# Kernel optimization log

Hardware: AMD Instinct MI355X
Metric: run time of the kernel (lower is better)

The kernel has to match this reference:

```python
import jax, jax.numpy as jnp
import numpy as np
import math

N_EMBD = 1024
N_HEAD = 16
HEAD_DIM = N_EMBD // N_HEAD // 2  # 32
DEPTH = 1
LAMBDA_INIT = 0.8 - 0.6 * math.exp(-0.3 * (DEPTH - 1))  # 0.2
EPS = 1e-5


def setup_inputs() -> dict:
    key = jax.random.key(0)
    ks = jax.random.split(key, 8)
    B, T, C = 4, 1024, N_EMBD
    x = jax.random.normal(ks[0], (B, T, C), dtype=jnp.float32)
    w_attn = jax.random.normal(ks[1], (C, 3 * C), dtype=jnp.float32) * (1.0 / math.sqrt(C))
    w_proj = jax.random.normal(ks[2], (C, C), dtype=jnp.float32) * (1.0 / math.sqrt(C))
    lambda_q1 = jax.random.normal(ks[3], (HEAD_DIM,), dtype=jnp.float32) * 0.1
    lambda_q2 = jax.random.normal(ks[4], (HEAD_DIM,), dtype=jnp.float32) * 0.1
    lambda_k1 = jax.random.normal(ks[5], (HEAD_DIM,), dtype=jnp.float32) * 0.1
    lambda_k2 = jax.random.normal(ks[6], (HEAD_DIM,), dtype=jnp.float32) * 0.1
    gamma = jnp.ones((2 * HEAD_DIM,), dtype=jnp.float32)  # RMSNorm affine weight
    return {"x": x, "w_attn": w_attn, "w_proj": w_proj,
            "lambda_q1": lambda_q1, "lambda_q2": lambda_q2,
            "lambda_k1": lambda_k1, "lambda_k2": lambda_k2, "gamma": gamma}


def reference(x, w_attn, w_proj, lambda_q1, lambda_q2, lambda_k1, lambda_k2, gamma):
    B, T, C = x.shape
    H, hd = N_HEAD, HEAD_DIM
    qkv = x @ w_attn                                  # [B,T,3C]
    q, k, v = jnp.split(qkv, 3, axis=-1)
    q = q.reshape(B, T, 2 * H, hd).transpose(0, 2, 1, 3)   # [B,2H,T,hd]
    k = k.reshape(B, T, 2 * H, hd).transpose(0, 2, 1, 3)   # [B,2H,T,hd]
    v = v.reshape(B, T, H, 2 * hd).transpose(0, 2, 1, 3)   # [B,H,T,2hd]
    q = q * (hd ** -0.5)
    att = jnp.einsum('bhtd,bhsd->bhts', q, k) * (1.0 / math.sqrt(hd))
    causal = jnp.tril(jnp.ones((T, T), dtype=bool))
    att = jnp.where(causal, att, -jnp.inf)
    att = jax.nn.softmax(att, axis=-1)                # [B,2H,T,T]
    lam1 = jnp.exp(jnp.sum(lambda_q1 * lambda_k1))
    lam2 = jnp.exp(jnp.sum(lambda_q2 * lambda_k2))
    lambda_full = lam1 - lam2 + LAMBDA_INIT
    att = att.reshape(B, H, 2, T, T)
    att = att[:, :, 0] - lambda_full * att[:, :, 1]   # [B,H,T,T]
    out = jnp.einsum('bhts,bhsd->bhtd', att, v)       # [B,H,T,2hd]
    # RMSNorm over last dim with affine weight
    rms = jax.lax.rsqrt(jnp.mean(out * out, axis=-1, keepdims=True) + EPS)
    out = out * rms * gamma
    out = (1.0 - LAMBDA_INIT) * out
    out = out.transpose(0, 2, 1, 3).reshape(B, T, C)
    return out @ w_proj
```

## Files before the change

### kernel.cpp

```cpp
#include <hip/hip_runtime.h>

typedef unsigned short u16;
typedef __bf16 bf16x8 __attribute__((ext_vector_type(8)));
typedef float f32x4 __attribute__((ext_vector_type(4)));
typedef u16 u16x8 __attribute__((ext_vector_type(8)));
typedef u16 u16x4 __attribute__((ext_vector_type(4)));

#define DEV static __device__ __forceinline__

DEV u16 f2bf(float f) {
  unsigned u = __builtin_bit_cast(unsigned, f);
  u += 0x7fffu + ((u >> 16) & 1u);
  return (u16)(u >> 16);
}
DEV u16 f2bf_fast(float f) {
  unsigned u = __builtin_bit_cast(unsigned, f);
  return (u16)((u + 0x8000u) >> 16);
}
DEV float fexp2(float x) {
  float r;
  asm("v_exp_f32 %0, %1" : "=v"(r) : "v"(x));
  return r;
}

DEV void gld16(const void* g, void* l) {
  __builtin_amdgcn_global_load_lds((__attribute__((address_space(1))) void*)(g),
                                   (__attribute__((address_space(3))) void*)(l),
                                   16, 0, 0);
}

__global__ __launch_bounds__(256) void k_cast(const float* __restrict__ in,
                                              u16* __restrict__ out, int n4) {
  int i = blockIdx.x * 256 + threadIdx.x;
  if (i >= n4) return;
  float4 v = ((const float4*)in)[i];
  u16x4 r = { f2bf(v.x), f2bf(v.y), f2bf(v.z), f2bf(v.w) };
  ((u16x4*)out)[i] = r;
}

__global__ __launch_bounds__(256) void k_transpose_cast(const float* __restrict__ in,
                                                        u16* __restrict__ out,
                                                        int R, int Cc) {
  __shared__ u16 tile[64][65];
  int r0 = blockIdx.x * 64, c0 = blockIdx.y * 64;
  int tid = threadIdx.x;
#pragma unroll
  for (int rr = 0; rr < 4; ++rr) {
    int r = rr * 16 + (tid >> 4);
    int c = (tid & 15) * 4;
    float4 v = *(const float4*)&in[(size_t)(r0 + r) * Cc + c0 + c];
    tile[r][c + 0] = f2bf(v.x); tile[r][c + 1] = f2bf(v.y);
    tile[r][c + 2] = f2bf(v.z); tile[r][c + 3] = f2bf(v.w);
  }
  __syncthreads();
#pragma unroll
  for (int rr = 0; rr < 2; ++rr) {
    int cr = rr * 32 + (tid >> 3);
    int rc = (tid & 7) * 8;
    u16x8 v;
#pragma unroll
    for (int j = 0; j < 8; ++j) v[j] = tile[rc + j][cr];
    *(u16x8*)&out[(size_t)(c0 + cr) * R + r0 + rc] = v;
  }
}

__global__ __launch_bounds__(256) void k_vtrans(const u16* __restrict__ qkv,
                                                u16* __restrict__ vt) {
  __shared__ u16 tile[64][65];
  int bid = blockIdx.x;
  int b = bid >> 8, h = (bid >> 4) & 15, tt = bid & 15;
  int tid = threadIdx.x;
#pragma unroll
  for (int rr = 0; rr < 2; ++rr) {
    int tl = rr * 32 + (tid >> 3);
    int d0 = (tid & 7) * 8;
    u16x8 v = *(const u16x8*)&qkv[(size_t)(b * 1024 + tt * 64 + tl) * 3072 + 2048 + h * 64 + d0];
#pragma unroll
    for (int j = 0; j < 8; ++j) tile[tl][d0 + j] = v[j];
  }
  __syncthreads();
#pragma unroll
  for (int rr = 0; rr < 2; ++rr) {
    int d = rr * 32 + (tid >> 3);
    int t0 = (tid & 7) * 8;
    u16x8 v;
#pragma unroll
    for (int j = 0; j < 8; ++j) v[j] = tile[t0 + j][d];
    *(u16x8*)&vt[((size_t)(b * 16 + h) * 64 + d) * 1024 + tt * 64 + t0] = v;
  }
}

__global__ void k_lambda(const float* lq1, const float* lq2,
                         const float* lk1, const float* lk2, float* out) {
  int i = threadIdx.x;
  float a = 0.f, b = 0.f;
  if (i < 32) { a = lq1[i] * lk1[i]; b = lq2[i] * lk2[i]; }
#pragma unroll
  for (int s = 1; s < 64; s <<= 1) { a += __shfl_xor(a, s); b += __shfl_xor(b, s); }
  if (i == 0) out[0] = __expf(a) - __expf(b) + 0.2f;
}

template <bool OUT_F32>
__global__ __launch_bounds__(256) void k_gemm(const u16* __restrict__ A,
                                              const u16* __restrict__ Bt,
                                              void* __restrict__ Cout,
                                              int M, int N, int K) {
  __shared__ __align__(16) u16 As[128 * 32];
  __shared__ __align__(16) u16 Bs[128 * 32];
  int tid = threadIdx.x;
  int nbn = N >> 7;
  int bm = blockIdx.x / nbn, bn = blockIdx.x % nbn;
  int m0 = bm << 7, n0 = bn << 7;
  int lane = tid & 63, w = tid >> 6, wm = w >> 1, wn = w & 1;
  int lr = lane & 15, lg = lane >> 4;
  f32x4 acc[4][4] = {};
  for (int kt = 0; kt < K; kt += 32) {
#pragma unroll
    for (int rr = 0; rr < 2; ++rr) {
      int i = rr * 256 + tid;
      int r = i >> 2, c8 = i & 3;
      int s8 = c8 ^ ((r >> 1) & 3);
      gld16(&A[(size_t)(m0 + r) * K + kt + s8 * 8], &As[i * 8]);
    }
#pragma unroll
    for (int rr = 0; rr < 2; ++rr) {
      int i = rr * 256 + tid;
      int r = i >> 2, c8 = i & 3;
      int s8 = c8 ^ ((r >> 1) & 3);
      gld16(&Bt[(size_t)(n0 + r) * K + kt + s8 * 8], &Bs[i * 8]);
    }
    __syncthreads();
    bf16x8 af[4], bfr[4];
#pragma unroll
    for (int m = 0; m < 4; ++m) {
      int r = wm * 64 + m * 16 + lr;
      int c8 = lg ^ ((r >> 1) & 3);
      af[m] = *(const bf16x8*)&As[r * 32 + c8 * 8];
    }
#pragma unroll
    for (int n = 0; n < 4; ++n) {
      int r = wn * 64 + n * 16 + lr;
      int c8 = lg ^ ((r >> 1) & 3);
      bfr[n] = *(const bf16x8*)&Bs[r * 32 + c8 * 8];
    }
#pragma unroll
    for (int m = 0; m < 4; ++m)
#pragma unroll
      for (int n = 0; n < 4; ++n)
        acc[m][n] = __builtin_amdgcn_mfma_f32_16x16x32_bf16(af[m], bfr[n], acc[m][n], 0, 0, 0);
    __syncthreads();
  }
#pragma unroll
  for (int m = 0; m < 4; ++m)
#pragma unroll
    for (int r = 0; r < 4; ++r) {
      int gr = m0 + wm * 64 + m * 16 + lg * 4 + r;
#pragma unroll
      for (int n = 0; n < 4; ++n) {
        int gc = n0 + wn * 64 + n * 16 + lr;
        if (OUT_F32) ((float*)Cout)[(size_t)gr * N + gc] = acc[m][n][r];
        else ((u16*)Cout)[(size_t)gr * N + gc] = f2bf(acc[m][n][r]);
      }
    }
}

__global__ __launch_bounds__(256) void k_diffattn(const u16* __restrict__ qkv,
                                                  const u16* __restrict__ vt,
                                                  const float* __restrict__ lam_p,
                                                  const float* __restrict__ gamma,
                                                  u16* __restrict__ attn_out) {
  __shared__ __align__(16) u16 Ks[2][2][64 * 32];
  __shared__ __align__(16) u16 Vs[2][64 * 64];
  __shared__ __align__(16) u16 Ps[4][2][16 * 72];
  int bid = blockIdx.x;
  int p = bid >> 6, b = (bid >> 4) & 3, h = bid & 15;
  int tid = threadIdx.x, lane = tid & 63, w = tid >> 6;
  int lr = lane & 15, lg = lane >> 4;
  int g1 = 2 * h, g2 = g1 + 1;
  float lam = *lam_p;
  const u16* vbase = vt + ((size_t)(b * 16 + h) * 64) * 1024;
  const float cexp = 0.045084222f;

  auto stage = [&](int s0, int buf) {
    int i = tid, r = i >> 2, c8 = i & 3;
    int s8 = c8 ^ ((r >> 1) & 3);
    size_t krow = (size_t)(b * 1024 + s0 + r) * 3072 + 1024;
    gld16(&qkv[krow + g1 * 32 + s8 * 8], &Ks[buf][0][i * 8]);
    gld16(&qkv[krow + g2 * 32 + s8 * 8], &Ks[buf][1][i * 8]);
#pragma unroll
    for (int rr = 0; rr < 2; ++rr) {
      int j = rr * 256 + tid;
      int d = j >> 3, o = (j & 7) ^ (d & 7);
      gld16(&vbase[(size_t)d * 1024 + s0 + o * 8], &Vs[buf][j * 8]);
    }
  };

  auto phase = [&](int qb) {
    int q0 = qb * 64;
    size_t qrow = (size_t)(b * 1024 + q0 + w * 16 + lr);
    bf16x8 qf1 = *(const bf16x8*)&qkv[qrow * 3072 + g1 * 32 + lg * 8];
    bf16x8 qf2 = *(const bf16x8*)&qkv[qrow * 3072 + g2 * 32 + lg * 8];
    f32x4 o1[4] = {}, o2[4] = {};
    float l1[4] = {}, l2[4] = {};
    u16* P1 = &Ps[w][0][0];
    u16* P2 = &Ps[w][1][0];
    int qg_base = q0 + w * 16 + lg * 4;
    int nt = qb + 1;
    f32x4 zero = {0.f, 0.f, 0.f, 0.f};

    stage(0, 0);
    for (int t = 0; t < nt; ++t) {
      int cur = t & 1;
      if (t + 1 < nt) {
        stage((t + 1) * 64, cur ^ 1);
        asm volatile("s_waitcnt vmcnt(4)" ::: "memory");
      } else {
        asm volatile("s_waitcnt vmcnt(0)" ::: "memory");
      }
      __builtin_amdgcn_s_barrier();
      __builtin_amdgcn_sched_barrier(0);

      int s0 = t * 64;
      bool diag = (t == qb);
      f32x4 s1[4], s2[4];
#pragma unroll
      for (int ni = 0; ni < 4; ++ni) {
        int rk = ni * 16 + lr;
        int c8 = lg ^ ((rk >> 1) & 3);
        bf16x8 kf1 = *(const bf16x8*)&Ks[cur][0][rk * 32 + c8 * 8];
        bf16x8 kf2 = *(const bf16x8*)&Ks[cur][1][rk * 32 + c8 * 8];
        s1[ni] = __builtin_amdgcn_mfma_f32_16x16x32_bf16(qf1, kf1, zero, 0, 0, 0);
        s2[ni] = __builtin_amdgcn_mfma_f32_16x16x32_bf16(qf2, kf2, zero, 0, 0, 0);
      }
#pragma unroll
      for (int ni = 0; ni < 4; ++ni) {
        int sg = s0 + ni * 16 + lr;
#pragma unroll
        for (int r = 0; r < 4; ++r) {
          float p1 = fexp2(s1[ni][r] * cexp);
          float p2 = fexp2(s2[ni][r] * cexp);
          if (diag && sg > qg_base + r) { p1 = 0.f; p2 = 0.f; }
          l1[r] += p1; l2[r] += p2;
          P1[(lg * 4 + r) * 72 + ni * 16 + lr] = f2bf_fast(p1);
          P2[(lg * 4 + r) * 72 + ni * 16 + lr] = f2bf_fast(p2);
        }
      }
#pragma unroll
      for (int kk = 0; kk < 2; ++kk) {
        bf16x8 pa1 = *(const bf16x8*)&P1[lr * 72 + kk * 32 + lg * 8];
        bf16x8 pa2 = *(const bf16x8*)&P2[lr * 72 + kk * 32 + lg * 8];
#pragma unroll
        for (int ni = 0; ni < 4; ++ni) {
          int d = ni * 16 + lr;
          int c8 = (kk * 4 + lg) ^ (d & 7);
          bf16x8 vb = *(const bf16x8*)&Vs[cur][d * 64 + c8 * 8];
          o1[ni] = __builtin_amdgcn_mfma_f32_16x16x32_bf16(pa1, vb, o1[ni], 0, 0, 0);
          o2[ni] = __builtin_amdgcn_mfma_f32_16x16x32_bf16(pa2, vb, o2[ni], 0, 0, 0);
        }
      }
      __builtin_amdgcn_sched_barrier(0);
      __builtin_amdgcn_s_barrier();
    }

#pragma unroll
    for (int r = 0; r < 4; ++r) {
      l1[r] += __shfl_xor(l1[r], 1); l1[r] += __shfl_xor(l1[r], 2);
      l1[r] += __shfl_xor(l1[r], 4); l1[r] += __shfl_xor(l1[r], 8);
      l2[r] += __shfl_xor(l2[r], 1); l2[r] += __shfl_xor(l2[r], 2);
      l2[r] += __shfl_xor(l2[r], 4); l2[r] += __shfl_xor(l2[r], 8);
    }
    float inv1[4], inv2[4];
#pragma unroll
    for (int r = 0; r < 4; ++r) { inv1[r] = 1.f / l1[r]; inv2[r] = 1.f / l2[r]; }
    float val[4][4];
#pragma unroll
    for (int ni = 0; ni < 4; ++ni)
#pragma unroll
      for (int r = 0; r < 4; ++r)
        val[ni][r] = o1[ni][r] * inv1[r] - lam * (o2[ni][r] * inv2[r]);
#pragma unroll
    for (int r = 0; r < 4; ++r) {
      float ss = 0.f;
#pragma unroll
      for (int ni = 0; ni < 4; ++ni) ss += val[ni][r] * val[ni][r];
      ss += __shfl_xor(ss, 1); ss += __shfl_xor(ss, 2);
      ss += __shfl_xor(ss, 4); ss += __shfl_xor(ss, 8);
      float sc = rsqrtf(ss * (1.f / 64.f) + 1e-5f) * 0.8f;
#pragma unroll
      for (int ni = 0; ni < 4; ++ni) val[ni][r] *= sc;
    }
#pragma unroll
    for (int ni = 0; ni < 4; ++ni) {
      int d = ni * 16 + lr;
      float g = gamma[d];
#pragma unroll
      for (int r = 0; r < 4; ++r) {
        int trow = q0 + w * 16 + lg * 4 + r;
        attn_out[(size_t)(b * 1024 + trow) * 1024 + h * 64 + d] = f2bf(val[ni][r] * g);
      }
    }
  };

  phase(p);
  __syncthreads();
  phase(15 - p);
}

extern "C" void kernel_launch(void* const* d_in, const int* in_sizes, int n_in,
                              void* d_out, int out_size, void* d_ws, size_t ws_size,
                              hipStream_t stream) {
  const float* x   = (const float*)d_in[0];
  const float* wa  = (const float*)d_in[1];
  const float* wp  = (const float*)d_in[2];
  const float* lq1 = (const float*)d_in[3];
  const float* lq2 = (const float*)d_in[4];
  const float* lk1 = (const float*)d_in[5];
  const float* lk2 = (const float*)d_in[6];
  const float* gam = (const float*)d_in[7];
  float* out = (float*)d_out;

  char* ws = (char*)d_ws;
  u16* xb   = (u16*)(ws);
  u16* wab  = (u16*)(ws + (8ull << 20));
  u16* wpb  = (u16*)(ws + (14ull << 20));
  u16* qkv  = (u16*)(ws + (16ull << 20));
  u16* vt   = (u16*)(ws + (40ull << 20));
  u16* aout = (u16*)(ws + (48ull << 20));
  float* lam = (float*)(ws + (56ull << 20));

  k_cast<<<4096, 256, 0, stream>>>(x, xb, 1024 * 1024);
  k_transpose_cast<<<dim3(16, 48), 256, 0, stream>>>(wa, wab, 1024, 3072);
  k_transpose_cast<<<dim3(16, 16), 256, 0, stream>>>(wp, wpb, 1024, 1024);
  k_lambda<<<1, 64, 0, stream>>>(lq1, lq2, lk1, lk2, lam);
  k_gemm<false><<<32 * 24, 256, 0, stream>>>(xb, wab, qkv, 4096, 3072, 1024);
  k_vtrans<<<1024, 256, 0, stream>>>(qkv, vt);
  k_diffattn<<<512, 256, 0, stream>>>(qkv, vt, lam, gam, aout);
  k_gemm<true><<<32 * 8, 256, 0, stream>>>(aout, wpb, out, 4096, 1024, 1024);
}
```

Measured before the change: 200.1 us.

## Double-buffer GEMM LDS loads, swizzle block order, precompute pointers, split masked attention tile

```diff
diff --git a/kernel.cpp b/kernel.cpp
--- a/kernel.cpp
+++ b/kernel.cpp
@@ -1,12 +1,16 @@
 #include <hip/hip_runtime.h>
 
 typedef unsigned short u16;
+typedef unsigned int u32;
 typedef __bf16 bf16x8 __attribute__((ext_vector_type(8)));
 typedef float f32x4 __attribute__((ext_vector_type(4)));
 typedef u16 u16x8 __attribute__((ext_vector_type(8)));
 typedef u16 u16x4 __attribute__((ext_vector_type(4)));
 
 #define DEV static __device__ __forceinline__
+
+struct MaskT { static constexpr bool value = true; };
+struct NoMaskT { static constexpr bool value = false; };
 
 DEV u16 f2bf(float f) {
   unsigned u = __builtin_bit_cast(unsigned, f);
@@ -105,50 +109,64 @@
                                               const u16* __restrict__ Bt,
                                               void* __restrict__ Cout,
                                               int M, int N, int K) {
-  __shared__ __align__(16) u16 As[128 * 32];
-  __shared__ __align__(16) u16 Bs[128 * 32];
+  __shared__ __align__(16) u16 As[2][128 * 32];
+  __shared__ __align__(16) u16 Bs[2][128 * 32];
   int tid = threadIdx.x;
   int nbn = N >> 7;
-  int bm = blockIdx.x / nbn, bn = blockIdx.x % nbn;
+  int wg = ((int)blockIdx.x & 7) * ((int)gridDim.x >> 3) + ((int)blockIdx.x >> 3);
+  int bm = wg / nbn, bn = wg % nbn;
   int m0 = bm << 7, n0 = bn << 7;
   int lane = tid & 63, w = tid >> 6, wm = w >> 1, wn = w & 1;
   int lr = lane & 15, lg = lane >> 4;
+  const u16* pA0; const u16* pA1; const u16* pB0; const u16* pB1;
+  {
+    int i0 = tid, i1 = tid + 256;
+    int r0 = i0 >> 2, s80 = (i0 & 3) ^ ((r0 >> 1) & 3);
+    int r1 = i1 >> 2, s81 = (i1 & 3) ^ ((r1 >> 1) & 3);
+    pA0 = &A[(size_t)(m0 + r0) * K + s80 * 8];
+    pA1 = &A[(size_t)(m0 + r1) * K + s81 * 8];
+    pB0 = &Bt[(size_t)(n0 + r0) * K + s80 * 8];
+    pB1 = &Bt[(size_t)(n0 + r1) * K + s81 * 8];
+  }
   f32x4 acc[4][4] = {};
-  for (int kt = 0; kt < K; kt += 32) {
-#pragma unroll
-    for (int rr = 0; rr < 2; ++rr) {
-      int i = rr * 256 + tid;
-      int r = i >> 2, c8 = i & 3;
-      int s8 = c8 ^ ((r >> 1) & 3);
-      gld16(&A[(size_t)(m0 + r) * K + kt + s8 * 8], &As[i * 8]);
-    }
-#pragma unroll
-    for (int rr = 0; rr < 2; ++rr) {
-      int i = rr * 256 + tid;
-      int r = i >> 2, c8 = i & 3;
-      int s8 = c8 ^ ((r >> 1) & 3);
-      gld16(&Bt[(size_t)(n0 + r) * K + kt + s8 * 8], &Bs[i * 8]);
-    }
-    __syncthreads();
+  auto stage = [&](int kt, int buf) {
+    gld16(pA0 + kt, &As[buf][tid * 8]);
+    gld16(pA1 + kt, &As[buf][(tid + 256) * 8]);
+    gld16(pB0 + kt, &Bs[buf][tid * 8]);
+    gld16(pB1 + kt, &Bs[buf][(tid + 256) * 8]);
+  };
+  int NK = K >> 5;
+  stage(0, 0);
+  for (int ki = 0; ki < NK; ++ki) {
+    int cur = ki & 1;
+    if (ki + 1 < NK) {
+      stage((ki + 1) << 5, cur ^ 1);
+      asm volatile("s_waitcnt vmcnt(4)" ::: "memory");
+    } else {
+      asm volatile("s_waitcnt vmcnt(0)" ::: "memory");
+    }
+    __builtin_amdgcn_s_barrier();
+    __builtin_amdgcn_sched_barrier(0);
     bf16x8 af[4], bfr[4];
 #pragma unroll
     for (int m = 0; m < 4; ++m) {
       int r = wm * 64 + m * 16 + lr;
       int c8 = lg ^ ((r >> 1) & 3);
-      af[m] = *(const bf16x8*)&As[r * 32 + c8 * 8];
+      af[m] = *(const bf16x8*)&As[cur][r * 32 + c8 * 8];
     }
 #pragma unroll
     for (int n = 0; n < 4; ++n) {
       int r = wn * 64 + n * 16 + lr;
       int c8 = lg ^ ((r >> 1) & 3);
-      bfr[n] = *(const bf16x8*)&Bs[r * 32 + c8 * 8];
+      bfr[n] = *(const bf16x8*)&Bs[cur][r * 32 + c8 * 8];
     }
 #pragma unroll
     for (int m = 0; m < 4; ++m)
 #pragma unroll
       for (int n = 0; n < 4; ++n)
         acc[m][n] = __builtin_amdgcn_mfma_f32_16x16x32_bf16(af[m], bfr[n], acc[m][n], 0, 0, 0);
-    __syncthreads();
+    __builtin_amdgcn_sched_barrier(0);
+    __builtin_amdgcn_s_barrier();
   }
 #pragma unroll
   for (int m = 0; m < 4; ++m)
@@ -178,21 +196,33 @@
   int lr = lane & 15, lg = lane >> 4;
   int g1 = 2 * h, g2 = g1 + 1;
   float lam = *lam_p;
-  const u16* vbase = vt + ((size_t)(b * 16 + h) * 64) * 1024;
   const float cexp = 0.045084222f;
+  f32x4 zero = {0.f, 0.f, 0.f, 0.f};
+  u16* P1 = &Ps[w][0][0];
+  u16* P2 = &Ps[w][1][0];
+
+  const u16* pK1; const u16* pK2;
+  {
+    int r = tid >> 2, c8 = tid & 3;
+    int s8 = c8 ^ ((r >> 1) & 3);
+    size_t krow = (size_t)(b * 1024 + r) * 3072 + 1024;
+    pK1 = qkv + krow + g1 * 32 + s8 * 8;
+    pK2 = qkv + krow + g2 * 32 + s8 * 8;
+  }
+  const u16* pV0; const u16* pV1;
+  {
+    const u16* vbase = vt + ((size_t)(b * 16 + h) * 64) * 1024;
+    int d0 = tid >> 3, o0 = (tid & 7) ^ (d0 & 7);
+    int d1 = d0 + 32;
+    pV0 = vbase + (size_t)d0 * 1024 + o0 * 8;
+    pV1 = vbase + (size_t)d1 * 1024 + o0 * 8;
+  }
 
   auto stage = [&](int s0, int buf) {
-    int i = tid, r = i >> 2, c8 = i & 3;
-    int s8 = c8 ^ ((r >> 1) & 3);
-    size_t krow = (size_t)(b * 1024 + s0 + r) * 3072 + 1024;
-    gld16(&qkv[krow + g1 * 32 + s8 * 8], &Ks[buf][0][i * 8]);
-    gld16(&qkv[krow + g2 * 32 + s8 * 8], &Ks[buf][1][i * 8]);
-#pragma unroll
-    for (int rr = 0; rr < 2; ++rr) {
-      int j = rr * 256 + tid;
-      int d = j >> 3, o = (j & 7) ^ (d & 7);
-      gld16(&vbase[(size_t)d * 1024 + s0 + o * 8], &Vs[buf][j * 8]);
-    }
+    gld16(pK1 + (size_t)s0 * 3072, &Ks[buf][0][tid * 8]);
+    gld16(pK2 + (size_t)s0 * 3072, &Ks[buf][1][tid * 8]);
+    gld16(pV0 + s0, &Vs[buf][tid * 8]);
+    gld16(pV1 + s0, &Vs[buf][(tid + 256) * 8]);
   };
 
   auto phase = [&](int qb) {
@@ -202,26 +232,9 @@
     bf16x8 qf2 = *(const bf16x8*)&qkv[qrow * 3072 + g2 * 32 + lg * 8];
     f32x4 o1[4] = {}, o2[4] = {};
     float l1[4] = {}, l2[4] = {};
-    u16* P1 = &Ps[w][0][0];
-    u16* P2 = &Ps[w][1][0];
     int qg_base = q0 + w * 16 + lg * 4;
-    int nt = qb + 1;
-    f32x4 zero = {0.f, 0.f, 0.f, 0.f};
-
-    stage(0, 0);
-    for (int t = 0; t < nt; ++t) {
-      int cur = t & 1;
-      if (t + 1 < nt) {
-        stage((t + 1) * 64, cur ^ 1);
-        asm volatile("s_waitcnt vmcnt(4)" ::: "memory");
-      } else {
-        asm volatile("s_waitcnt vmcnt(0)" ::: "memory");
-      }
-      __builtin_amdgcn_s_barrier();
-      __builtin_amdgcn_sched_barrier(0);
-
-      int s0 = t * 64;
-      bool diag = (t == qb);
+
+    auto tile = [&](int cur, int s0, auto mk) {
       f32x4 s1[4], s2[4];
 #pragma unroll
       for (int ni = 0; ni < 4; ++ni) {
@@ -237,12 +250,14 @@
         int sg = s0 + ni * 16 + lr;
 #pragma unroll
         for (int r = 0; r < 4; ++r) {
-          float p1 = fexp2(s1[ni][r] * cexp);
-          float p2 = fexp2(s2[ni][r] * cexp);
-          if (diag && sg > qg_base + r) { p1 = 0.f; p2 = 0.f; }
-          l1[r] += p1; l2[r] += p2;
-          P1[(lg * 4 + r) * 72 + ni * 16 + lr] = f2bf_fast(p1);
-          P2[(lg * 4 + r) * 72 + ni * 16 + lr] = f2bf_fast(p2);
+          float v1 = fexp2(s1[ni][r] * cexp);
+          float v2 = fexp2(s2[ni][r] * cexp);
+          if constexpr (decltype(mk)::value) {
+            if (sg > qg_base + r) { v1 = 0.f; v2 = 0.f; }
+          }
+          l1[r] += v1; l2[r] += v2;
+          P1[(lg * 4 + r) * 72 + ni * 16 + lr] = f2bf_fast(v1);
+          P2[(lg * 4 + r) * 72 + ni * 16 + lr] = f2bf_fast(v2);
         }
       }
 #pragma unroll
@@ -258,9 +273,23 @@
           o2[ni] = __builtin_amdgcn_mfma_f32_16x16x32_bf16(pa2, vb, o2[ni], 0, 0, 0);
         }
       }
+    };
+
+    stage(0, 0);
+    for (int t = 0; t < qb; ++t) {
+      int cur = t & 1;
+      stage((t + 1) * 64, cur ^ 1);
+      asm volatile("s_waitcnt vmcnt(4)" ::: "memory");
+      __builtin_amdgcn_s_barrier();
+      __builtin_amdgcn_sched_barrier(0);
+      tile(cur, t * 64, NoMaskT{});
       __builtin_amdgcn_sched_barrier(0);
       __builtin_amdgcn_s_barrier();
     }
+    asm volatile("s_waitcnt vmcnt(0)" ::: "memory");
+    __builtin_amdgcn_s_barrier();
+    __builtin_amdgcn_sched_barrier(0);
+    tile(qb & 1, q0, MaskT{});
 
 #pragma unroll
     for (int r = 0; r < 4; ++r) {
```

Result: faster. 191.4 us (-4.4%).
